# Optimization experiments

Hardware: AMD Instinct MI355X
Metric: run time of the kernel (lower is better)

The kernel has to match this reference:

```python
import jax, jax.numpy as jnp
from jax import lax
import numpy as np

LATENT = 256
FLAT = 128 * 28 * 28  # 100352


def _conv(x, w, b, stride):
    # PyTorch Conv2d(k=3, stride, padding=1) in NCHW/OIHW
    y = lax.conv_general_dilated(x, w, (stride, stride), ((1, 1), (1, 1)),
                                 dimension_numbers=('NCHW', 'OIHW', 'NCHW'))
    return y + b[None, :, None, None]


def _deconv(x, w, b):
    # PyTorch ConvTranspose2d(k=3, stride=2, padding=1, output_padding=1).
    # w has PyTorch layout [in, out, kh, kw]; flip spatially + swap io -> OIHW.
    wt = jnp.flip(w, (2, 3)).transpose(1, 0, 2, 3)
    y = lax.conv_general_dilated(x, wt, (1, 1), ((1, 2), (1, 2)),
                                 lhs_dilation=(2, 2),
                                 dimension_numbers=('NCHW', 'OIHW', 'NCHW'))
    return y + b[None, :, None, None]


def _self_attn(x, wq, bq, wk, bk, wv, bv, gamma):
    # Full spatial self-attention over N = H*W tokens (the headroom hotspot).
    B, C, H, W = x.shape
    N = H * W
    xf = x.reshape(B, C, N)
    q = jnp.einsum('oc,bcn->bno', wq, xf) + bq            # [B, N, C//8]
    k = jnp.einsum('oc,bcn->bon', wk, xf) + bk[None, :, None]  # [B, C//8, N]
    attn = jax.nn.softmax(jnp.einsum('bno,bom->bnm', q, k), axis=-1)  # [B,N,N]
    v = jnp.einsum('oc,bcn->bon', wv, xf) + bv[None, :, None]  # [B, C, N]
    out = jnp.einsum('bcn,bmn->bcm', v, attn).reshape(B, C, H, W)
    return gamma * out + x


def setup_inputs() -> dict:
    key = jax.random.key(0)
    ks = iter(jax.random.split(key, 40))
    n = lambda shape, s=0.05: jax.random.normal(next(ks), shape, dtype=jnp.float32) * s
    inp = {
        'x': jax.random.normal(next(ks), (1, 3, 224, 224), dtype=jnp.float32),
        'eps': jax.random.normal(next(ks), (1, LATENT), dtype=jnp.float32),
        'conv1_w': n((32, 3, 3, 3)), 'conv1_b': n((32,)),
        'q1_w': n((4, 32)), 'q1_b': n((4,)),
        'k1_w': n((4, 32)), 'k1_b': n((4,)),
        'v1_w': n((32, 32)), 'v1_b': n((32,)),
        'gamma1': jnp.full((1,), 0.1, dtype=jnp.float32),
        'conv2_w': n((64, 32, 3, 3)), 'conv2_b': n((64,)),
        'q2_w': n((8, 64)), 'q2_b': n((8,)),
        'k2_w': n((8, 64)), 'k2_b': n((8,)),
        'v2_w': n((64, 64)), 'v2_b': n((64,)),
        'gamma2': jnp.full((1,), 0.1, dtype=jnp.float32),
        'conv3_w': n((128, 64, 3, 3)), 'conv3_b': n((128,)),
        'fc_mu_w': n((FLAT, LATENT), 0.01), 'fc_mu_b': n((LATENT,)),
        'fc_lv_w': n((FLAT, LATENT), 0.01), 'fc_lv_b': n((LATENT,)),
        'fc_dec_w': n((LATENT, FLAT), 0.01), 'fc_dec_b': n((FLAT,)),
        'dc1_w': n((128, 64, 3, 3)), 'dc1_b': n((64,)),
        'dc2_w': n((64, 32, 3, 3)), 'dc2_b': n((32,)),
        'dc3_w': n((32, 3, 3, 3)), 'dc3_b': n((3,)),
    }
    return inp


def reference(x, eps, conv1_w, conv1_b, q1_w, q1_b, k1_w, k1_b, v1_w, v1_b, gamma1,
              conv2_w, conv2_b, q2_w, q2_b, k2_w, k2_b, v2_w, v2_b, gamma2,
              conv3_w, conv3_b, fc_mu_w, fc_mu_b, fc_lv_w, fc_lv_b,
              fc_dec_w, fc_dec_b, dc1_w, dc1_b, dc2_w, dc2_b, dc3_w, dc3_b):
    B = x.shape[0]
    h = jax.nn.relu(_conv(x, conv1_w, conv1_b, 2))          # [B,32,112,112]
    h = _self_attn(h, q1_w, q1_b, k1_w, k1_b, v1_w, v1_b, gamma1)
    h = jax.nn.relu(_conv(h, conv2_w, conv2_b, 2))          # [B,64,56,56]
    h = _self_attn(h, q2_w, q2_b, k2_w, k2_b, v2_w, v2_b, gamma2)
    h = jax.nn.relu(_conv(h, conv3_w, conv3_b, 2))          # [B,128,28,28]
    hf = h.reshape(B, FLAT)
    mu = hf @ fc_mu_w + fc_mu_b
    logvar = hf @ fc_lv_w + fc_lv_b
    z = mu + eps * jnp.exp(0.5 * logvar)                    # reparametrize
    d = jax.nn.relu(z @ fc_dec_w + fc_dec_b).reshape(B, 128, 28, 28)
    d = jax.nn.relu(_deconv(d, dc1_w, dc1_b))               # [B,64,56,56]
    d = jax.nn.relu(_deconv(d, dc2_w, dc2_b))               # [B,32,112,112]
    recon = jax.nn.sigmoid(_deconv(d, dc3_w, dc3_b))        # [B,3,224,224]
    return recon, mu, logvar
```

## Files before the change

### kernel.cpp

```cpp
#include <hip/hip_runtime.h>
#include <hip/hip_bf16.h>

typedef __hip_bfloat16 bf16;
typedef __attribute__((ext_vector_type(8))) short short8v;
typedef __attribute__((ext_vector_type(4))) float f32x4;

__device__ __forceinline__ unsigned int cvtpk(float lo, float hi){
  unsigned int r;
  asm("v_cvt_pk_bf16_f32 %0, %1, %2" : "=v"(r) : "v"(lo), "v"(hi));
  return r;
}
__device__ __forceinline__ float exp2a(float x){
  float r;
  asm("v_exp_f32 %0, %1" : "=v"(r) : "v"(x));
  return r;
}
__device__ __forceinline__ float blo(unsigned u){ return __uint_as_float(u<<16); }
__device__ __forceinline__ float bhi(unsigned u){ return __uint_as_float(u & 0xffff0000u); }

template<int CIN>
__global__ __launch_bounds__(256) void k_conv_s2t(const float* __restrict__ in, const float* __restrict__ w,
    const float* __restrict__ bias, float* __restrict__ out, int Hin, int Win){
  const int Hout = Hin>>1, Wout = Win>>1, HW = Hout*Wout;
  __shared__ float wl[CIN*9];
  const int oc = blockIdx.y, tid = threadIdx.x;
  for(int i=tid;i<CIN*9;i+=256) wl[i] = w[oc*CIN*9 + i];
  __syncthreads();
  const int idx = blockIdx.x*256 + tid;
  if(idx >= HW) return;
  const int oy = idx/Wout, ox = idx - oy*Wout;
  const int iy0 = 2*oy-1, ix0 = 2*ox-1;
  const float mt = iy0>=0 ? 1.f:0.f, ml = ix0>=0 ? 1.f:0.f;
  const int iyc = iy0<0?0:iy0, ixc = ix0<0?0:ix0;
  const int x1 = ix0+1, x2 = ix0+2;
  float acc = bias[oc];
  #pragma unroll 4
  for(int ic=0; ic<CIN; ++ic){
    const float* b0 = in + (ic*Hin + iyc )*Win;
    const float* b1 = in + (ic*Hin + iy0+1)*Win;
    const float* b2 = in + (ic*Hin + iy0+2)*Win;
    const float* wp = wl + ic*9;
    float t00 = b0[ixc]*(mt*ml), t01 = b0[x1]*mt, t02 = b0[x2]*mt;
    float t10 = b1[ixc]*ml,      t11 = b1[x1],    t12 = b1[x2];
    float t20 = b2[ixc]*ml,      t21 = b2[x1],    t22 = b2[x2];
    acc += t00*wp[0]+t01*wp[1]+t02*wp[2]
         + t10*wp[3]+t11*wp[4]+t12*wp[5]
         + t20*wp[6]+t21*wp[7]+t22*wp[8];
  }
  out[oc*HW + idx] = fmaxf(acc, 0.f);
}

template<int C, int O, int TPN>
__global__ __launch_bounds__(256) void k_qkv(const float* __restrict__ x,
    const float* __restrict__ wq, const float* __restrict__ bq,
    const float* __restrict__ wk, const float* __restrict__ bk,
    const float* __restrict__ wv, const float* __restrict__ bv,
    float* __restrict__ q, float* __restrict__ k, bf16* __restrict__ v, int N){
  constexpr int NPB = 256/TPN;
  constexpr int OP = O/TPN > 0 ? O/TPN : 1;
  constexpr int CP = C/TPN;
  const int n = blockIdx.x*NPB + threadIdx.x/TPN;
  const int p = threadIdx.x%TPN;
  float xc[C];
  #pragma unroll
  for(int c=0;c<C;++c) xc[c] = x[c*N+n];
  #pragma unroll
  for(int oo=0;oo<OP;++oo){
    int o = p*OP + oo;
    float aq = bq[o], ak = bk[o];
    #pragma unroll
    for(int c=0;c<C;++c){ aq += wq[o*C+c]*xc[c]; ak += wk[o*C+c]*xc[c]; }
    q[n*O+o] = aq;
    k[o*N+n] = ak;
  }
  #pragma unroll
  for(int cc=0;cc<CP;++cc){
    int o = p*CP + cc;
    float av = bv[o];
    #pragma unroll
    for(int c=0;c<C;++c) av += wv[o*C+c]*xc[c];
    v[o*N+n] = __float2bfloat16(av);
  }
}

template<int C, int O, int ST, int NSPLIT, int QG>
__global__ __launch_bounds__(256) void k_attn_mfma(
    const float* __restrict__ q, const float* __restrict__ kk, const bf16* __restrict__ vb,
    float* __restrict__ pacc, float* __restrict__ pden, int N){
  constexpr int NT = C/16;
  constexpr int OH = O/2;
  constexpr int VROW = ST*2 + 16;
  constexpr int VIT  = C*(ST/8)/256;
  __shared__ __align__(16) char vsm[2][C*VROW];
  __shared__ unsigned int ksmu[2][(ST + ST/8)*OH];
  const int tid = threadIdx.x;
  const int qblk = blockIdx.x / NSPLIT, split = blockIdx.x % NSPLIT;
  const int KEYS = N / NSPLIT;
  const int kbase = split * KEYS;
  const int wv = tid >> 6;
  const int l  = tid & 63;
  const int lg = l >> 4, lq = l & 15;
  const int qbase = qblk*(64*QG) + wv*(16*QG);
  float qv[QG][O];
  #pragma unroll
  for(int g=0; g<QG; ++g)
    #pragma unroll
    for(int o=0;o<O;++o) qv[g][o] = q[(qbase + g*16 + lq)*O + o] * 1.44269504f;
  f32x4 acc[QG][NT];
  #pragma unroll
  for(int g=0; g<QG; ++g)
    #pragma unroll
    for(int nt=0;nt<NT;++nt) acc[g][nt] = (f32x4){0.f,0.f,0.f,0.f};
  float den[QG];
  #pragma unroll
  for(int g=0; g<QG; ++g) den[g] = 0.f;

  unsigned int kregu[OH];
  uint4  vreg[VIT];
  const bool kact = tid < ST;

  auto LOAD = [&](int g0){
    if(kact){
      #pragma unroll
      for(int h=0;h<OH;++h)
        kregu[h] = cvtpk(kk[(2*h+0)*N + kbase + g0 + tid],
                         kk[(2*h+1)*N + kbase + g0 + tid]);
    }
    #pragma unroll
    for(int i=0;i<VIT;++i){
      int ch = i*256 + tid;
      int c = ch/(ST/8), j8 = ch%(ST/8);
      vreg[i] = *(const uint4*)(vb + (size_t)c*N + kbase + g0 + j8*8);
    }
  };
  auto STORE = [&](int b){
    if(kact){
      int row = tid + (tid>>3);
      if constexpr(O==4){
        *(uint2*)&ksmu[b][row*OH] = make_uint2(kregu[0], kregu[1]);
      } else {
        *(uint4*)&ksmu[b][row*OH] = make_uint4(kregu[0], kregu[1], kregu[2], kregu[3]);
      }
    }
    #pragma unroll
    for(int i=0;i<VIT;++i){
      int ch = i*256 + tid;
      int c = ch/(ST/8), j8 = ch%(ST/8);
      *(uint4*)(vsm[b] + c*VROW + j8*16) = vreg[i];
    }
  };

  const int NTILE = KEYS/ST;
  LOAD(0);
  STORE(0);
  __syncthreads();
  int cur = 0;
  for(int t=0; t<NTILE; ++t){
    if(t+1 < NTILE) LOAD((t+1)*ST);
    #pragma unroll
    for(int s=0; s<ST/32; ++s){
      float pr[QG][8];
      #pragma unroll
      for(int e=0; e<8; ++e){
        const int row = s*36 + lg*9 + e;
        unsigned kw[OH];
        if constexpr(O==4){
          uint2 t2 = *(const uint2*)&ksmu[cur][row*OH];
          kw[0]=t2.x; kw[1]=t2.y;
        } else {
          uint4 t4 = *(const uint4*)&ksmu[cur][row*OH];
          kw[0]=t4.x; kw[1]=t4.y; kw[2]=t4.z; kw[3]=t4.w;
        }
        float kf[O];
        #pragma unroll
        for(int h=0;h<OH;++h){ kf[2*h]=blo(kw[h]); kf[2*h+1]=bhi(kw[h]); }
        #pragma unroll
        for(int g=0; g<QG; ++g){
          float sc = 0.f;
          #pragma unroll
          for(int o=0;o<O;++o) sc = fmaf(qv[g][o], kf[o], sc);
          pr[g][e] = exp2a(sc);
        }
      }
      union { unsigned int u[4]; short8v s8; } pa[QG];
      #pragma unroll
      for(int g=0; g<QG; ++g){
        #pragma unroll
        for(int u=0; u<4; ++u) pa[g].u[u] = cvtpk(pr[g][2*u], pr[g][2*u+1]);
        #pragma unroll
        for(int e=0; e<8; ++e) den[g] += pr[g][e];
      }
      #pragma unroll
      for(int nt=0; nt<NT; ++nt){
        short8v bf_ = *(const short8v*)(vsm[cur] + (lq + nt*16)*VROW + (s*32 + lg*8)*2);
        #pragma unroll
        for(int g=0; g<QG; ++g)
          acc[g][nt] = __builtin_amdgcn_mfma_f32_16x16x32_bf16(pa[g].s8, bf_, acc[g][nt], 0,0,0);
      }
    }
    if(t+1 < NTILE) STORE(cur^1);
    __syncthreads();
    cur ^= 1;
  }
  #pragma unroll
  for(int g=0; g<QG; ++g){
    den[g] += __shfl_xor(den[g], 16);
    den[g] += __shfl_xor(den[g], 32);
    if(lg == 0) pden[(size_t)split*N + qbase + g*16 + lq] = den[g];
  }
  #pragma unroll
  for(int g=0; g<QG; ++g)
    #pragma unroll
    for(int nt=0; nt<NT; ++nt)
      #pragma unroll
      for(int r=0;r<4;++r){
        int qg_ = qbase + g*16 + lg*4 + r;
        pacc[((size_t)split*N + qg_)*C + nt*16 + lq] = acc[g][nt][r];
      }
}

template<int C, int NSPLIT>
__global__ __launch_bounds__(256) void k_attn_combT(const float* __restrict__ pacc,
    const float* __restrict__ pden, const float* __restrict__ xin,
    const float* __restrict__ gamma, float* __restrict__ out, int N){
  __shared__ float tl[C][65];
  __shared__ float dl[64];
  const int t = threadIdx.x;
  const int m0 = blockIdx.x*64;
  if(t < 64){
    float d = 0.f;
    #pragma unroll
    for(int s=0;s<NSPLIT;++s) d += pden[(size_t)s*N + m0 + t];
    dl[t] = d;
  }
  constexpr int E = 64*C/256;
  #pragma unroll
  for(int e=0;e<E;++e){
    int f = e*256 + t;
    int ml = f/C, c = f - ml*C;
    float a = 0.f;
    #pragma unroll
    for(int s=0;s<NSPLIT;++s) a += pacc[(size_t)s*N*C + (size_t)m0*C + f];
    tl[c][ml] = a;
  }
  __syncthreads();
  const float gm = gamma[0];
  #pragma unroll
  for(int e=0;e<E;++e){
    int f = e*256 + t;
    int c = f>>6, ml = f & 63;
    size_t gi = (size_t)c*N + m0 + ml;
    out[gi] = gm * tl[c][ml] / dl[ml] + xin[gi];
  }
}

__global__ __launch_bounds__(256) void k_fc2_part(const float* __restrict__ hf,
    const float* __restrict__ wmu, const float* __restrict__ wlv,
    float* __restrict__ pmu, float* __restrict__ plv){
  __shared__ float sh[64];
  __shared__ f32x4 red[4][64];
  const int t = threadIdx.x, blk = blockIdx.x, f0 = blk*64;
  const int w = t>>6, l = t&63;
  const float* wsel = blockIdx.y ? wlv : wmu;
  float*       dsel = blockIdx.y ? plv : pmu;
  if(t < 64) sh[t] = hf[f0+t];
  __syncthreads();
  const f32x4* wp = (const f32x4*)(wsel + (size_t)(f0 + w*16)*256) + l;
  f32x4 a = {0.f,0.f,0.f,0.f};
  #pragma unroll
  for(int r=0; r<16; ++r){
    float h = sh[w*16 + r];
    f32x4 u = __builtin_nontemporal_load(&wp[r*64]);
    a += h*u;
  }
  red[w][l] = a;
  __syncthreads();
  const float* rr = (const float*)red;
  dsel[(size_t)blk*256 + t] = rr[t] + rr[256+t] + rr[512+t] + rr[768+t];
}

__global__ __launch_bounds__(256) void k_reparam_p(const float* __restrict__ pmu, const float* __restrict__ plv,
    const float* __restrict__ bmu, const float* __restrict__ blv, const float* __restrict__ eps,
    float* __restrict__ z, float* __restrict__ omu, float* __restrict__ olv){
  const int o = blockIdx.x, t = threadIdx.x;
  __shared__ float rm[4], rl[4];
  float sm = 0.f, sl = 0.f;
  for(int j=t; j<1568; j+=256){ sm += pmu[(size_t)j*256+o]; sl += plv[(size_t)j*256+o]; }
  #pragma unroll
  for(int off=32; off>=1; off>>=1){ sm += __shfl_xor(sm, off); sl += __shfl_xor(sl, off); }
  if((t&63)==0){ rm[t>>6]=sm; rl[t>>6]=sl; }
  __syncthreads();
  if(t==0){
    float mu = bmu[o] + rm[0]+rm[1]+rm[2]+rm[3];
    float lv = blv[o] + rl[0]+rl[1]+rl[2]+rl[3];
    z[o] = mu + eps[o] * expf(0.5f*lv);
    omu[o] = mu;
    olv[o] = lv;
  }
}

template<int OSPL>
__global__ __launch_bounds__(256) void k_fc_dec_p(const float* __restrict__ z, const float* __restrict__ w,
    float* __restrict__ pfd){
  constexpr int OPC = 256/OSPL;
  __shared__ float sz[OPC];
  const int t = threadIdx.x, blk = blockIdx.x, os = blockIdx.y;
  if(t<OPC) sz[t] = z[os*OPC + t];
  __syncthreads();
  const size_t f4 = (size_t)blk*256 + t;
  const f32x4* wp = (const f32x4*)w + (size_t)os*OPC*25088 + f4;
  f32x4 a = {0.f,0.f,0.f,0.f};
  #pragma unroll 8
  for(int o=0;o<OPC;++o){
    float zz = sz[o];
    f32x4 u = __builtin_nontemporal_load(&wp[(size_t)o*25088]);
    a += zz*u;
  }
  ((f32x4*)pfd)[(size_t)os*25088 + f4] = a;
}

template<int OSPL>
__global__ __launch_bounds__(256) void k_fc_dec_c(const float* __restrict__ pfd, const float* __restrict__ b,
    float* __restrict__ out){
  const int i = blockIdx.x*256 + threadIdx.x;
  const f32x4* p4 = (const f32x4*)pfd;
  f32x4 s = ((const f32x4*)b)[i];
  #pragma unroll
  for(int k=0;k<OSPL;++k) s += p4[(size_t)k*25088 + i];
  s[0]=fmaxf(s[0],0.f); s[1]=fmaxf(s[1],0.f); s[2]=fmaxf(s[2],0.f); s[3]=fmaxf(s[3],0.f);
  ((f32x4*)out)[i] = s;
}

template<int CIN, int COUT, int ACT>
__global__ __launch_bounds__(256) void k_deconv_p(const float* __restrict__ in, const float* __restrict__ w,
    const float* __restrict__ bias, float* __restrict__ out, int Hin, int Win){
  __shared__ float wl[CIN*9];
  const int oc = blockIdx.y;
  const int tid = threadIdx.x;
  for(int i=tid; i<CIN*9; i+=256) wl[i] = w[((i/9)*COUT + oc)*9 + (i%9)];
  __syncthreads();
  const int nq = Hin*Win;
  const int code = blockIdx.x*256 + tid;
  if(code >= 4*nq) return;
  const int q = code % nq;
  const int pcode = code / nq;
  const int px = pcode & 1, py = pcode >> 1;
  const int qy = q / Win, qx = q - qy*Win;
  const float m1x = (qx+1 < Win) ? 1.f : 0.f;
  const float m1y = (qy+1 < Hin) ? 1.f : 0.f;
  const int qxc = (qx+1 < Win) ? qx+1 : qx;
  const int qyc = (qy+1 < Hin) ? qy+1 : qy;
  const int o00 = qy*Win+qx, o01 = qy*Win+qxc, o10 = qyc*Win+qx, o11 = qyc*Win+qxc;
  const int HW = nq;
  float acc = bias[oc];
  if(pcode == 0){
    #pragma unroll 4
    for(int ic=0; ic<CIN; ++ic) acc += in[ic*HW + o00] * wl[ic*9+4];
  } else if(pcode == 1){
    #pragma unroll 4
    for(int ic=0; ic<CIN; ++ic){
      acc += in[ic*HW + o00] * wl[ic*9+5];
      acc += (in[ic*HW + o01]*m1x) * wl[ic*9+3];
    }
  } else if(pcode == 2){
    #pragma unroll 4
    for(int ic=0; ic<CIN; ++ic){
      acc += in[ic*HW + o00] * wl[ic*9+7];
      acc += (in[ic*HW + o10]*m1y) * wl[ic*9+1];
    }
  } else {
    #pragma unroll 4
    for(int ic=0; ic<CIN; ++ic){
      acc += in[ic*HW + o00] * wl[ic*9+8];
      acc += (in[ic*HW + o01]*m1x) * wl[ic*9+6];
      acc += (in[ic*HW + o10]*m1y) * wl[ic*9+2];
      acc += (in[ic*HW + o11]*(m1x*m1y)) * wl[ic*9+0];
    }
  }
  const int oy = 2*qy+py, ox = 2*qx+px;
  float r = (ACT==0) ? fmaxf(acc, 0.f) : 1.f/(1.f + __expf(-acc));
  out[(oc*2*Hin + oy)*2*Win + ox] = r;
}

extern "C" void kernel_launch(void* const* d_in, const int* in_sizes, int n_in,
                              void* d_out, int out_size, void* d_ws, size_t ws_size,
                              hipStream_t stream){
  const float* X    = (const float*)d_in[0];
  const float* EPS  = (const float*)d_in[1];
  const float* c1w  = (const float*)d_in[2];  const float* c1b = (const float*)d_in[3];
  const float* q1w  = (const float*)d_in[4];  const float* q1b = (const float*)d_in[5];
  const float* k1w  = (const float*)d_in[6];  const float* k1b = (const float*)d_in[7];
  const float* v1w  = (const float*)d_in[8];  const float* v1b = (const float*)d_in[9];
  const float* g1   = (const float*)d_in[10];
  const float* c2w  = (const float*)d_in[11]; const float* c2b = (const float*)d_in[12];
  const float* q2w  = (const float*)d_in[13]; const float* q2b = (const float*)d_in[14];
  const float* k2w  = (const float*)d_in[15]; const float* k2b = (const float*)d_in[16];
  const float* v2w  = (const float*)d_in[17]; const float* v2b = (const float*)d_in[18];
  const float* g2   = (const float*)d_in[19];
  const float* c3w  = (const float*)d_in[20]; const float* c3b = (const float*)d_in[21];
  const float* fmw  = (const float*)d_in[22]; const float* fmb = (const float*)d_in[23];
  const float* flw  = (const float*)d_in[24]; const float* flb = (const float*)d_in[25];
  const float* fdw  = (const float*)d_in[26]; const float* fdb = (const float*)d_in[27];
  const float* d1w  = (const float*)d_in[28]; const float* d1b = (const float*)d_in[29];
  const float* d2w  = (const float*)d_in[30]; const float* d2b = (const float*)d_in[31];
  const float* d3w  = (const float*)d_in[32]; const float* d3b = (const float*)d_in[33];

  float* ws  = (float*)d_ws;
  float* h1  = ws;
  float* h1a = h1  + 401408;
  float* q1  = h1a + 401408;
  float* k1  = q1  + 50176;
  float* v1f = k1  + 50176;
  float* h2  = v1f + 401408;
  float* h2a = h2  + 200704;
  float* q2  = h2a + 200704;
  float* k2  = q2  + 25088;
  float* v2f = k2  + 25088;
  float* h3  = v2f + 200704;
  float* z   = h3  + 100352 + 200704;
  float* part= h3  + 100352 + 200704 + 256;
  bf16* v1b_ = (bf16*)v1f;
  bf16* v2b_ = (bf16*)v2f;
  float* pmu = part;
  float* plv = part + 401408;
  float* pfd = part + 802816;
  float* dd0 = h1;
  float* dd1 = h1 + 100352;
  float* dd2 = h1a;

  const size_t base = 2258176;
  const bool big = ws_size >= (base + 2809856 + 87808) * 4;
  float* pdn = part + (big ? 2809856 : 802816);

  float* OUT = (float*)d_out;

  k_conv_s2t<3><<<dim3(49,32),dim3(256),0,stream>>>(X, c1w, c1b, h1, 224, 224);
  k_qkv<32,4,4><<<dim3(196),dim3(256),0,stream>>>(h1, q1w,q1b, k1w,k1b, v1w,v1b, q1,k1,v1b_, 12544);
  if(big){
    k_attn_mfma<32,4,128,7,2><<<dim3(686),dim3(256),0,stream>>>(q1,k1,v1b_, part, pdn, 12544);
    k_attn_combT<32,7><<<dim3(196),dim3(256),0,stream>>>(part, pdn, h1, g1, h1a, 12544);
  } else {
    k_attn_mfma<32,4,128,2,2><<<dim3(196),dim3(256),0,stream>>>(q1,k1,v1b_, part, pdn, 12544);
    k_attn_combT<32,2><<<dim3(196),dim3(256),0,stream>>>(part, pdn, h1, g1, h1a, 12544);
  }
  k_conv_s2t<32><<<dim3(13,64),dim3(256),0,stream>>>(h1a, c2w, c2b, h2, 112, 112);
  k_qkv<64,8,8><<<dim3(98),dim3(256),0,stream>>>(h2, q2w,q2b, k2w,k2b, v2w,v2b, q2,k2,v2b_, 3136);
  if(big){
    k_attn_mfma<64,8,64,7,1><<<dim3(343),dim3(256),0,stream>>>(q2,k2,v2b_, part, pdn, 3136);
    k_attn_combT<64,7><<<dim3(49),dim3(256),0,stream>>>(part, pdn, h2, g2, h2a, 3136);
  } else {
    k_attn_mfma<64,8,64,1,1><<<dim3(49),dim3(256),0,stream>>>(q2,k2,v2b_, part, pdn, 3136);
    k_attn_combT<64,1><<<dim3(49),dim3(256),0,stream>>>(part, pdn, h2, g2, h2a, 3136);
  }
  k_conv_s2t<64><<<dim3(4,128),dim3(256),0,stream>>>(h2a, c3w, c3b, h3, 56, 56);
  k_fc2_part<<<dim3(1568,2),dim3(256),0,stream>>>(h3, fmw, flw, pmu, plv);
  k_reparam_p<<<dim3(256),dim3(256),0,stream>>>(pmu, plv, fmb, flb, EPS, z, OUT+150528, OUT+150784);
  if(big){
    k_fc_dec_p<16><<<dim3(98,16),dim3(256),0,stream>>>(z, fdw, pfd);
    k_fc_dec_c<16><<<dim3(98),dim3(256),0,stream>>>(pfd, fdb, dd0);
  } else {
    k_fc_dec_p<4><<<dim3(98,4),dim3(256),0,stream>>>(z, fdw, pfd);
    k_fc_dec_c<4><<<dim3(98),dim3(256),0,stream>>>(pfd, fdb, dd0);
  }
  k_deconv_p<128,64,0><<<dim3(13,64),dim3(256),0,stream>>>(dd0, d1w, d1b, dd1, 28,28);
  k_deconv_p<64,32,0><<<dim3(49,32),dim3(256),0,stream>>>(dd1, d2w, d2b, dd2, 56,56);
  k_deconv_p<32,3,1><<<dim3(196,3),dim3(256),0,stream>>>(dd2, d3w, d3b, OUT, 112,112);
}
```

Measured before the change: 348.1 us.

## Add 14-way key split for first attention and fuse mu/logvar FC blocks

```diff
diff --git a/kernel.cpp b/kernel.cpp
--- a/kernel.cpp
+++ b/kernel.cpp
@@ -258,25 +258,30 @@
     const float* __restrict__ wmu, const float* __restrict__ wlv,
     float* __restrict__ pmu, float* __restrict__ plv){
   __shared__ float sh[64];
-  __shared__ f32x4 red[4][64];
+  __shared__ f32x4 redm[4][64];
+  __shared__ f32x4 redl[4][64];
   const int t = threadIdx.x, blk = blockIdx.x, f0 = blk*64;
   const int w = t>>6, l = t&63;
-  const float* wsel = blockIdx.y ? wlv : wmu;
-  float*       dsel = blockIdx.y ? plv : pmu;
   if(t < 64) sh[t] = hf[f0+t];
   __syncthreads();
-  const f32x4* wp = (const f32x4*)(wsel + (size_t)(f0 + w*16)*256) + l;
-  f32x4 a = {0.f,0.f,0.f,0.f};
+  const f32x4* wpm = (const f32x4*)(wmu + (size_t)(f0 + w*16)*256) + l;
+  const f32x4* wpl = (const f32x4*)(wlv + (size_t)(f0 + w*16)*256) + l;
+  f32x4 am = {0.f,0.f,0.f,0.f}, al = {0.f,0.f,0.f,0.f};
   #pragma unroll
   for(int r=0; r<16; ++r){
     float h = sh[w*16 + r];
-    f32x4 u = __builtin_nontemporal_load(&wp[r*64]);
-    a += h*u;
-  }
-  red[w][l] = a;
-  __syncthreads();
-  const float* rr = (const float*)red;
-  dsel[(size_t)blk*256 + t] = rr[t] + rr[256+t] + rr[512+t] + rr[768+t];
+    f32x4 um = __builtin_nontemporal_load(&wpm[r*64]);
+    f32x4 ul = __builtin_nontemporal_load(&wpl[r*64]);
+    am += h*um;
+    al += h*ul;
+  }
+  redm[w][l] = am;
+  redl[w][l] = al;
+  __syncthreads();
+  const float* rm = (const float*)redm;
+  const float* rl = (const float*)redl;
+  pmu[(size_t)blk*256 + t] = rm[t] + rm[256+t] + rm[512+t] + rm[768+t];
+  plv[(size_t)blk*256 + t] = rl[t] + rl[256+t] + rl[512+t] + rl[768+t];
 }
 
 __global__ __launch_bounds__(256) void k_reparam_p(const float* __restrict__ pmu, const float* __restrict__ plv,
@@ -429,14 +434,18 @@
   float* dd2 = h1a;
 
   const size_t base = 2258176;
-  const bool big = ws_size >= (base + 2809856 + 87808) * 4;
-  float* pdn = part + (big ? 2809856 : 802816);
+  const bool huge = ws_size >= (base + 5619712 + 175616) * 4;
+  const bool big  = ws_size >= (base + 2809856 +  87808) * 4;
+  float* pdn = part + (huge ? 5619712 : big ? 2809856 : 802816);
 
   float* OUT = (float*)d_out;
 
   k_conv_s2t<3><<<dim3(49,32),dim3(256),0,stream>>>(X, c1w, c1b, h1, 224, 224);
   k_qkv<32,4,4><<<dim3(196),dim3(256),0,stream>>>(h1, q1w,q1b, k1w,k1b, v1w,v1b, q1,k1,v1b_, 12544);
-  if(big){
+  if(huge){
+    k_attn_mfma<32,4,128,14,2><<<dim3(1372),dim3(256),0,stream>>>(q1,k1,v1b_, part, pdn, 12544);
+    k_attn_combT<32,14><<<dim3(196),dim3(256),0,stream>>>(part, pdn, h1, g1, h1a, 12544);
+  } else if(big){
     k_attn_mfma<32,4,128,7,2><<<dim3(686),dim3(256),0,stream>>>(q1,k1,v1b_, part, pdn, 12544);
     k_attn_combT<32,7><<<dim3(196),dim3(256),0,stream>>>(part, pdn, h1, g1, h1a, 12544);
   } else {
@@ -445,7 +454,7 @@
   }
   k_conv_s2t<32><<<dim3(13,64),dim3(256),0,stream>>>(h1a, c2w, c2b, h2, 112, 112);
   k_qkv<64,8,8><<<dim3(98),dim3(256),0,stream>>>(h2, q2w,q2b, k2w,k2b, v2w,v2b, q2,k2,v2b_, 3136);
-  if(big){
+  if(big || huge){
     k_attn_mfma<64,8,64,7,1><<<dim3(343),dim3(256),0,stream>>>(q2,k2,v2b_, part, pdn, 3136);
     k_attn_combT<64,7><<<dim3(49),dim3(256),0,stream>>>(part, pdn, h2, g2, h2a, 3136);
   } else {
@@ -453,9 +462,9 @@
     k_attn_combT<64,1><<<dim3(49),dim3(256),0,stream>>>(part, pdn, h2, g2, h2a, 3136);
   }
   k_conv_s2t<64><<<dim3(4,128),dim3(256),0,stream>>>(h2a, c3w, c3b, h3, 56, 56);
-  k_fc2_part<<<dim3(1568,2),dim3(256),0,stream>>>(h3, fmw, flw, pmu, plv);
+  k_fc2_part<<<dim3(1568),dim3(256),0,stream>>>(h3, fmw, flw, pmu, plv);
   k_reparam_p<<<dim3(256),dim3(256),0,stream>>>(pmu, plv, fmb, flb, EPS, z, OUT+150528, OUT+150784);
-  if(big){
+  if(big || huge){
     k_fc_dec_p<16><<<dim3(98,16),dim3(256),0,stream>>>(z, fdw, pfd);
     k_fc_dec_c<16><<<dim3(98),dim3(256),0,stream>>>(pfd, fdb, dd0);
   } else {
```

Result: slower. 370.6 us (+6.4%).
